# Optimization experiments

Hardware: AMD Instinct MI355X
Metric: run time of the kernel (lower is better)

The kernel has to match this reference:

```python
import jax, jax.numpy as jnp
import numpy as np

N_NODES = 100000
IN_DIM = 128
HID = 128
N_REL = 2
N_EDGES = 500000


def setup_inputs() -> dict:
    key = jax.random.key(0)
    ks = jax.random.split(key, 12)
    x = jax.random.normal(ks[0], (N_NODES, IN_DIM), dtype=jnp.float32)
    edge_index = jax.random.randint(ks[1], (2, N_EDGES), 0, N_NODES, dtype=jnp.int64)
    edge_type = jax.random.randint(ks[2], (N_EDGES,), 0, N_REL, dtype=jnp.int64)
    def w(k, shape, fan_in):
        return jax.random.normal(k, shape, dtype=jnp.float32) / np.sqrt(fan_in)
    return {
        "x": x,
        "edge_index": edge_index,
        "edge_type": edge_type,
        "W_rel1": w(ks[3], (N_REL, IN_DIM, HID), IN_DIM),
        "W_root1": w(ks[4], (IN_DIM, HID), IN_DIM),
        "b1": jnp.zeros((HID,), jnp.float32),
        "W_rel2": w(ks[5], (N_REL, HID, HID), HID),
        "W_root2": w(ks[6], (HID, HID), HID),
        "b2": jnp.zeros((HID,), jnp.float32),
        "Wc": w(ks[7], (HID, 2), HID),
        "bc": jnp.zeros((2,), jnp.float32),
    }


def rgcn_conv(x, src, dst, edge_type, W_rel, W_root, b, n_nodes):
    """PyG RGCNConv: out_i = x_i @ W_root + b + sum_r mean_{j in N_r(i)} x_j @ W_r."""
    out = x @ W_root + b
    for r in range(W_rel.shape[0]):  # small fixed relation count
        mask = (edge_type == r).astype(x.dtype)  # [E]
        xr = x @ W_rel[r]                         # [N, dout] transform-then-gather
        msg = xr[src] * mask[:, None]             # [E, dout]
        agg = jax.ops.segment_sum(msg, dst, num_segments=n_nodes)   # [N, dout]
        cnt = jax.ops.segment_sum(mask, dst, num_segments=n_nodes)  # [N]
        out = out + agg / jnp.maximum(cnt, 1.0)[:, None]            # mean aggr
    return out


def reference(x, edge_index, edge_type, W_rel1, W_root1, b1, W_rel2, W_root2, b2, Wc, bc):
    n = x.shape[0]
    src, dst = edge_index[0], edge_index[1]
    h = rgcn_conv(x, src, dst, edge_type, W_rel1, W_root1, b1, n)
    h = jax.nn.relu(h)
    # dropout is identity at inference (training=False)
    h = rgcn_conv(h, src, dst, edge_type, W_rel2, W_root2, b2, n)
    h = jax.nn.relu(h)
    logits = h @ Wc + bc
    return logits
```

## Files before the change

kernel.cpp:

```cpp
#include <hip/hip_runtime.h>
#include <hip/hip_fp16.h>

#define N_NODES 100000
#define PAD_N   100096
#define IN_DIM 128
#define HID 128
#define N_REL 2
#define N_EDGES 500000
#define M_SEG (N_REL * N_NODES)
#define SCAN_BLK 1024
#define SCAN_NB ((M_SEG + SCAN_BLK - 1) / SCAN_BLK)

#define CVT_BLOCKS 12500
#define PACK_BLOCKS 48
#define HIST_BLOCKS 1954

typedef __attribute__((ext_vector_type(8))) _Float16 half8;
typedef __attribute__((ext_vector_type(4))) float float4v;

__device__ __forceinline__ unsigned short f2h(float f) {
    return __half_as_ushort(__float2half(f));
}

__global__ __launch_bounds__(256) void prep_kernel(
    const float* __restrict__ X, unsigned short* __restrict__ Xb,
    const float* __restrict__ Wroot1, const float* __restrict__ Wrel1,
    const float* __restrict__ Wroot2, const float* __restrict__ Wrel2,
    unsigned short* __restrict__ Wp,
    const int* __restrict__ ei, const int* __restrict__ et,
    unsigned* __restrict__ cnt)
{
    int bid = blockIdx.x;
    if (bid < CVT_BLOCKS) {
        int i = bid * 256 + threadIdx.x;
        if (i >= N_NODES * IN_DIM / 4) return;
        float4 v = ((const float4*)X)[i];
        ushort4 o;
        o.x = f2h(v.x); o.y = f2h(v.y); o.z = f2h(v.z); o.w = f2h(v.w);
        ((ushort4*)Xb)[i] = o;
    } else if (bid < CVT_BLOCKS + PACK_BLOCKS) {
        int tid = (bid - CVT_BLOCKS) * 256 + threadIdx.x;
        int layer = tid / 6144;
        int rem   = tid % 6144;
        int ks    = rem / 512;
        int rem2  = rem % 512;
        int nt    = rem2 / 64;
        int lane  = rem2 % 64;
        int seg = ks >> 2;
        int kl  = (ks & 3) * 32 + (lane >> 4) * 8;
        int chan = nt * 16 + (lane & 15);
        const float* Wroot = layer ? Wroot2 : Wroot1;
        const float* Wrel  = layer ? Wrel2  : Wrel1;
        const float* W = (seg == 0) ? Wroot : (Wrel + (size_t)(seg - 1) * 128 * 128);
        unsigned short* dst = Wp + (size_t)tid * 8;
        #pragma unroll
        for (int j = 0; j < 8; ++j)
            dst[j] = f2h(W[(size_t)(kl + j) * 128 + chan]);
    } else {
        int e = (bid - CVT_BLOCKS - PACK_BLOCKS) * 256 + threadIdx.x;
        if (e >= N_EDGES) return;
        int dst = ei[N_EDGES + e];
        int r = et[e];
        atomicAdd(cnt + (size_t)r * N_NODES + dst, 1u);
    }
}

__global__ __launch_bounds__(256) void scan1_kernel(
    const unsigned* __restrict__ cnt,
    unsigned* __restrict__ rs, unsigned* __restrict__ bsums)
{
    __shared__ unsigned sdata[256];
    int t = threadIdx.x;
    int base = blockIdx.x * SCAN_BLK + t * 4;
    unsigned v[4]; unsigned s = 0;
    #pragma unroll
    for (int j = 0; j < 4; ++j) {
        v[j] = (base + j < M_SEG) ? cnt[base + j] : 0u;
        s += v[j];
    }
    sdata[t] = s;
    __syncthreads();
    #pragma unroll
    for (int off = 1; off < 256; off <<= 1) {
        unsigned x = (t >= off) ? sdata[t - off] : 0u;
        __syncthreads();
        if (t >= off) sdata[t] += x;
        __syncthreads();
    }
    unsigned excl = (t > 0) ? sdata[t - 1] : 0u;
    if (t == 255) bsums[blockIdx.x] = sdata[255];
    unsigned run = excl;
    #pragma unroll
    for (int j = 0; j < 4; ++j) {
        if (base + j < M_SEG) rs[base + j] = run;
        run += v[j];
    }
}

__global__ __launch_bounds__(256) void scan2_kernel(unsigned* __restrict__ bsums)
{
    __shared__ unsigned sdata[256];
    int t = threadIdx.x;
    sdata[t] = (t < SCAN_NB) ? bsums[t] : 0u;
    __syncthreads();
    #pragma unroll
    for (int off = 1; off < 256; off <<= 1) {
        unsigned x = (t >= off) ? sdata[t - off] : 0u;
        __syncthreads();
        if (t >= off) sdata[t] += x;
        __syncthreads();
    }
    if (t < SCAN_NB) bsums[t] = (t > 0) ? sdata[t - 1] : 0u;
}

__global__ __launch_bounds__(256) void scan3_kernel(
    unsigned* __restrict__ rs, const unsigned* __restrict__ bsums,
    unsigned* __restrict__ cursor)
{
    int i = blockIdx.x * blockDim.x + threadIdx.x;
    if (i < M_SEG) {
        unsigned v = rs[i] + bsums[i >> 10];
        rs[i] = v;
        cursor[i] = v;
    }
    if (i == 0) rs[M_SEG] = N_EDGES;
}

__global__ __launch_bounds__(256) void fill_kernel(
    const int* __restrict__ ei, const int* __restrict__ et,
    unsigned* __restrict__ cursor, unsigned* __restrict__ csr)
{
    int e = blockIdx.x * blockDim.x + threadIdx.x;
    if (e >= N_EDGES) return;
    int src = ei[e];
    int dst = ei[N_EDGES + e];
    int r = et[e];
    unsigned pos = atomicAdd(cursor + (size_t)r * N_NODES + dst, 1u);
    csr[pos] = (unsigned)src;
}

template <bool FINAL>
__global__ __launch_bounds__(256) void gemm_kernel(
    const unsigned short* __restrict__ Xin,
    const unsigned* __restrict__ rs,
    const unsigned* __restrict__ csr,
    const unsigned short* __restrict__ Wp,
    const float* __restrict__ bias,
    unsigned short* __restrict__ Hout,
    const float* __restrict__ Wc,
    const float* __restrict__ bc,
    float* __restrict__ Out)
{
    const int t    = threadIdx.x;
    const int w    = t >> 6;
    const int lane = t & 63;
    const int l15  = lane & 15;
    const int quad = lane >> 4;
    const int rowbase = blockIdx.x * 128 + w * 32;
    const int koff = quad * 8;

    const uint4* __restrict__ X4 = (const uint4*)Xin;

    unsigned p_[4], e_[4]; float inv_[4];
    #pragma unroll
    for (int r = 0; r < 2; ++r) {
        #pragma unroll
        for (int mt = 0; mt < 2; ++mt) {
            int c = r * 2 + mt;
            int node = rowbase + mt * 16 + l15;
            unsigned st = 0, en = 0;
            if (node < N_NODES) {
                unsigned sg = (unsigned)r * N_NODES + (unsigned)node;
                st = rs[sg];
                en = rs[sg + 1];
            }
            p_[c] = st; e_[c] = en;
            unsigned cdeg = en - st;
            inv_[c] = 1.0f / (float)(cdeg > 0u ? cdeg : 1u);
        }
    }

    __half2 a2[4][4][4];
    #pragma unroll
    for (int c = 0; c < 4; ++c)
        #pragma unroll
        for (int ksl = 0; ksl < 4; ++ksl)
            #pragma unroll
            for (int j = 0; j < 4; ++j)
                a2[c][ksl][j] = __float2half2_rn(0.f);

    const __half2 one2  = __float2half2_rn(1.f);
    const __half2 zero2 = __float2half2_rn(0.f);

    while (true) {
        bool act[4];
        bool anyl = false;
        #pragma unroll
        for (int c = 0; c < 4; ++c) { act[c] = p_[c] < e_[c]; anyl |= act[c]; }
        if (!__any(anyl)) break;

        unsigned s_[4];
        #pragma unroll
        for (int c = 0; c < 4; ++c)
            s_[c] = csr[act[c] ? p_[c] : 0u];

        uint4 v_[4][4];
        #pragma unroll
        for (int c = 0; c < 4; ++c) {
            const uint4* row = X4 + ((size_t)(act[c] ? s_[c] : 0u) << 4) + quad;
            v_[c][0] = row[0];
            v_[c][1] = row[4];
            v_[c][2] = row[8];
            v_[c][3] = row[12];
        }

        #pragma unroll
        for (int c = 0; c < 4; ++c) {
            __half2 m = act[c] ? one2 : zero2;
            #pragma unroll
            for (int ksl = 0; ksl < 4; ++ksl)
                #pragma unroll
                for (int j = 0; j < 4; ++j)
                    a2[c][ksl][j] = __hfma2(((const __half2*)&v_[c][ksl])[j], m,
                                            a2[c][ksl][j]);
            p_[c] += act[c] ? 1u : 0u;
        }
    }

    half8 ag[2][2][4];
    #pragma unroll
    for (int r = 0; r < 2; ++r)
        #pragma unroll
        for (int mt = 0; mt < 2; ++mt) {
            int c = r * 2 + mt;
            __half2 s2 = __float2half2_rn(inv_[c]);
            #pragma unroll
            for (int ksl = 0; ksl < 4; ++ksl) {
                half8 h;
                #pragma unroll
                for (int j = 0; j < 4; ++j)
                    ((__half2*)&h)[j] = __hmul2(a2[c][ksl][j], s2);
                ag[r][mt][ksl] = h;
            }
        }

    auto ldB = [&](int ks, int nt) -> half8 {
        return *(const half8*)(Wp + ((size_t)(ks * 8 + nt) * 64 + lane) * 8);
    };
    const unsigned short* aBase0 = Xin + (size_t)(rowbase + l15) * 128 + koff;
    const unsigned short* aBase1 = aBase0 + 16 * 128;
    auto ldA = [&](int ks, int mt) -> half8 {
        return *(const half8*)((mt ? aBase1 : aBase0) + (ks & 3) * 32);
    };

    float4v acc[2][8];
    #pragma unroll
    for (int nt = 0; nt < 8; ++nt) {
        float bv = bias[nt * 16 + l15];
        #pragma unroll
        for (int mt = 0; mt < 2; ++mt)
            acc[mt][nt] = float4v{bv, bv, bv, bv};
    }

    half8 bb[2][8];
    half8 aa[2][2];
    #pragma unroll
    for (int nt = 0; nt < 8; ++nt) bb[0][nt] = ldB(0, nt);
    aa[0][0] = ldA(0, 0);
    aa[0][1] = ldA(0, 1);

    #pragma unroll
    for (int ks = 0; ks < 12; ++ks) {
        if (ks + 1 < 12) {
            #pragma unroll
            for (int nt = 0; nt < 8; ++nt)
                bb[(ks + 1) & 1][nt] = ldB(ks + 1, nt);
            if (ks + 1 < 4) {
                aa[(ks + 1) & 1][0] = ldA(ks + 1, 0);
                aa[(ks + 1) & 1][1] = ldA(ks + 1, 1);
            }
        }
        half8 A0 = (ks < 4) ? aa[ks & 1][0] : ag[(ks >> 2) - 1][0][ks & 3];
        half8 A1 = (ks < 4) ? aa[ks & 1][1] : ag[(ks >> 2) - 1][1][ks & 3];
        #pragma unroll
        for (int nt = 0; nt < 8; ++nt) {
            acc[0][nt] = __builtin_amdgcn_mfma_f32_16x16x32_f16(A0, bb[ks & 1][nt], acc[0][nt], 0, 0, 0);
            acc[1][nt] = __builtin_amdgcn_mfma_f32_16x16x32_f16(A1, bb[ks & 1][nt], acc[1][nt], 0, 0, 0);
        }
    }

    if (!FINAL) {
        #pragma unroll
        for (int mt = 0; mt < 2; ++mt) {
            #pragma unroll
            for (int r = 0; r < 4; ++r) {
                int node = rowbase + mt * 16 + quad * 4 + r;
                unsigned short* hp = Hout + (size_t)node * 128 + l15;
                #pragma unroll
                for (int nt = 0; nt < 8; ++nt)
                    hp[nt * 16] = f2h(fmaxf(acc[mt][nt][r], 0.f));
            }
        }
    } else {
        float wc0[8], wc1[8];
        #pragma unroll
        for (int nt = 0; nt < 8; ++nt) {
            wc0[nt] = Wc[(nt * 16 + l15) * 2 + 0];
            wc1[nt] = Wc[(nt * 16 + l15) * 2 + 1];
        }
        float b0 = bc[0], b1 = bc[1];
        #pragma unroll
        for (int mt = 0; mt < 2; ++mt) {
            #pragma unroll
            for (int r = 0; r < 4; ++r) {
                float l0 = 0.f, l1 = 0.f;
                #pragma unroll
                for (int nt = 0; nt < 8; ++nt) {
                    float h = fmaxf(acc[mt][nt][r], 0.f);
                    l0 += h * wc0[nt];
                    l1 += h * wc1[nt];
                }
                #pragma unroll
                for (int off = 8; off > 0; off >>= 1) {
                    l0 += __shfl_down(l0, off, 16);
                    l1 += __shfl_down(l1, off, 16);
                }
                int node = rowbase + mt * 16 + quad * 4 + r;
                if (l15 == 0 && node < N_NODES) {
                    Out[(size_t)node * 2 + 0] = l0 + b0;
                    Out[(size_t)node * 2 + 1] = l1 + b1;
                }
            }
        }
    }
}

extern "C" void kernel_launch(void* const* d_in, const int* in_sizes, int n_in,
                              void* d_out, int out_size, void* d_ws, size_t ws_size,
                              hipStream_t stream)
{
    const float* x      = (const float*)d_in[0];
    const int*   ei     = (const int*)d_in[1];
    const int*   et     = (const int*)d_in[2];
    const float* Wrel1  = (const float*)d_in[3];
    const float* Wroot1 = (const float*)d_in[4];
    const float* b1     = (const float*)d_in[5];
    const float* Wrel2  = (const float*)d_in[6];
    const float* Wroot2 = (const float*)d_in[7];
    const float* b2     = (const float*)d_in[8];
    const float* Wc     = (const float*)d_in[9];
    const float* bc     = (const float*)d_in[10];
    float* out = (float*)d_out;

    char* ws = (char*)d_ws;
    size_t off = 0;
    auto alloc = [&](size_t bytes) {
        void* p = ws + off;
        off += (bytes + 255) & ~(size_t)255;
        return p;
    };
    unsigned short* xb    = (unsigned short*)alloc((size_t)PAD_N * IN_DIM * 2);
    unsigned short* h1b   = (unsigned short*)alloc((size_t)PAD_N * HID * 2);
    unsigned short* Wp    = (unsigned short*)alloc((size_t)2 * 12 * 8 * 64 * 8 * 2);
    unsigned*       rs    = (unsigned*)alloc((size_t)(M_SEG + 1) * 4);
    unsigned*       cursor= (unsigned*)alloc((size_t)M_SEG * 4);
    unsigned*       bsums = (unsigned*)alloc(256 * 4);
    unsigned*       csr   = (unsigned*)alloc((size_t)N_EDGES * 4);

    const int edge_blocks = (N_EDGES + 255) / 256;
    const int seg_blocks  = (M_SEG + 255) / 256;
    const int gemm_blocks = PAD_N / 128;
    const int prep_blocks = CVT_BLOCKS + PACK_BLOCKS + HIST_BLOCKS;

    hipMemsetAsync(cursor, 0, (size_t)M_SEG * 4, stream);
    prep_kernel<<<prep_blocks, 256, 0, stream>>>(
        x, xb, Wroot1, Wrel1, Wroot2, Wrel2, Wp, ei, et, cursor);
    scan1_kernel<<<SCAN_NB, 256, 0, stream>>>(cursor, rs, bsums);
    scan2_kernel<<<1, 256, 0, stream>>>(bsums);
    scan3_kernel<<<seg_blocks, 256, 0, stream>>>(rs, bsums, cursor);
    fill_kernel<<<edge_blocks, 256, 0, stream>>>(ei, et, cursor, csr);

    gemm_kernel<false><<<gemm_blocks, 256, 0, stream>>>(
        xb, rs, csr, Wp, b1, h1b, nullptr, nullptr, nullptr);

    gemm_kernel<true><<<gemm_blocks, 256, 0, stream>>>(
        h1b, rs, csr, Wp + (size_t)12 * 8 * 64 * 8, b2, nullptr, Wc, bc, out);
}
```

Before: 271.3 us.

## Halve rows per warp and software-pipeline CSR index loads in gather loop

Each warp now handles 16 nodes instead of 32, doubling the number of gemm blocks, and the neighbor-gather loop processes two edges per relation per iteration while prefetching the next iteration's CSR indices. This is meant to cut per-warp load imbalance and register pressure and to hide the dependent csr-then-row load latency. The cost is that each B weight fragment is reused by one MFMA tile instead of two, which doubles weight traffic per node, and wasted lanes can rise on odd degrees.

```diff
diff --git a/kernel.cpp b/kernel.cpp
--- a/kernel.cpp
+++ b/kernel.cpp
@@ -156,118 +156,138 @@
     const int lane = t & 63;
     const int l15  = lane & 15;
     const int quad = lane >> 4;
-    const int rowbase = blockIdx.x * 128 + w * 32;
+    const int rowbase = blockIdx.x * 64 + w * 16;
     const int koff = quad * 8;
 
     const uint4* __restrict__ X4 = (const uint4*)Xin;
 
-    unsigned p_[4], e_[4]; float inv_[4];
+    const int node = rowbase + l15;
+    unsigned p_[2], e_[2]; float inv_[2];
     #pragma unroll
     for (int r = 0; r < 2; ++r) {
-        #pragma unroll
-        for (int mt = 0; mt < 2; ++mt) {
-            int c = r * 2 + mt;
-            int node = rowbase + mt * 16 + l15;
-            unsigned st = 0, en = 0;
-            if (node < N_NODES) {
-                unsigned sg = (unsigned)r * N_NODES + (unsigned)node;
-                st = rs[sg];
-                en = rs[sg + 1];
-            }
-            p_[c] = st; e_[c] = en;
-            unsigned cdeg = en - st;
-            inv_[c] = 1.0f / (float)(cdeg > 0u ? cdeg : 1u);
-        }
-    }
-
-    __half2 a2[4][4][4];
-    #pragma unroll
-    for (int c = 0; c < 4; ++c)
+        unsigned st = 0, en = 0;
+        if (node < N_NODES) {
+            unsigned sg = (unsigned)r * N_NODES + (unsigned)node;
+            st = rs[sg];
+            en = rs[sg + 1];
+        }
+        p_[r] = st; e_[r] = en;
+        unsigned d = en - st;
+        inv_[r] = 1.0f / (float)(d ? d : 1u);
+    }
+
+    __half2 a2[2][4][4];
+    #pragma unroll
+    for (int r = 0; r < 2; ++r)
         #pragma unroll
         for (int ksl = 0; ksl < 4; ++ksl)
             #pragma unroll
             for (int j = 0; j < 4; ++j)
-                a2[c][ksl][j] = __float2half2_rn(0.f);
+                a2[r][ksl][j] = __float2half2_rn(0.f);
 
     const __half2 one2  = __float2half2_rn(1.f);
     const __half2 zero2 = __float2half2_rn(0.f);
 
-    while (true) {
-        bool act[4];
-        bool anyl = false;
-        #pragma unroll
-        for (int c = 0; c < 4; ++c) { act[c] = p_[c] < e_[c]; anyl |= act[c]; }
-        if (!__any(anyl)) break;
-
-        unsigned s_[4];
-        #pragma unroll
-        for (int c = 0; c < 4; ++c)
-            s_[c] = csr[act[c] ? p_[c] : 0u];
-
-        uint4 v_[4][4];
-        #pragma unroll
-        for (int c = 0; c < 4; ++c) {
-            const uint4* row = X4 + ((size_t)(act[c] ? s_[c] : 0u) << 4) + quad;
-            v_[c][0] = row[0];
-            v_[c][1] = row[4];
-            v_[c][2] = row[8];
-            v_[c][3] = row[12];
-        }
-
-        #pragma unroll
-        for (int c = 0; c < 4; ++c) {
-            __half2 m = act[c] ? one2 : zero2;
-            #pragma unroll
-            for (int ksl = 0; ksl < 4; ++ksl)
+    unsigned id[2][2];
+    #pragma unroll
+    for (int r = 0; r < 2; ++r)
+        #pragma unroll
+        for (int s = 0; s < 2; ++s) {
+            unsigned q = p_[r] + (unsigned)s;
+            id[r][s] = csr[q < e_[r] ? q : 0u];
+        }
+
+    while (__any((p_[0] < e_[0]) | (p_[1] < e_[1]))) {
+        bool act[2][2];
+        #pragma unroll
+        for (int r = 0; r < 2; ++r)
+            #pragma unroll
+            for (int s = 0; s < 2; ++s)
+                act[r][s] = (p_[r] + (unsigned)s) < e_[r];
+
+        uint4 v[2][2][4];
+        #pragma unroll
+        for (int r = 0; r < 2; ++r)
+            #pragma unroll
+            for (int s = 0; s < 2; ++s) {
+                const uint4* row = X4 +
+                    ((size_t)(act[r][s] ? id[r][s] : 0u) << 4) + quad;
+                v[r][s][0] = row[0];
+                v[r][s][1] = row[4];
+                v[r][s][2] = row[8];
+                v[r][s][3] = row[12];
+            }
+
+        unsigned pn[2];
+        #pragma unroll
+        for (int r = 0; r < 2; ++r) {
+            unsigned q = p_[r] + 2u;
+            pn[r] = q > e_[r] ? e_[r] : q;
+        }
+        unsigned idn[2][2];
+        #pragma unroll
+        for (int r = 0; r < 2; ++r)
+            #pragma unroll
+            for (int s = 0; s < 2; ++s) {
+                unsigned q = pn[r] + (unsigned)s;
+                idn[r][s] = csr[q < e_[r] ? q : 0u];
+            }
+
+        #pragma unroll
+        for (int r = 0; r < 2; ++r)
+            #pragma unroll
+            for (int s = 0; s < 2; ++s) {
+                __half2 m = act[r][s] ? one2 : zero2;
                 #pragma unroll
-                for (int j = 0; j < 4; ++j)
-                    a2[c][ksl][j] = __hfma2(((const __half2*)&v_[c][ksl])[j], m,
-                                            a2[c][ksl][j]);
-            p_[c] += act[c] ? 1u : 0u;
-        }
-    }
-
-    half8 ag[2][2][4];
-    #pragma unroll
-    for (int r = 0; r < 2; ++r)
-        #pragma unroll
-        for (int mt = 0; mt < 2; ++mt) {
-            int c = r * 2 + mt;
-            __half2 s2 = __float2half2_rn(inv_[c]);
-            #pragma unroll
-            for (int ksl = 0; ksl < 4; ++ksl) {
-                half8 h;
-                #pragma unroll
-                for (int j = 0; j < 4; ++j)
-                    ((__half2*)&h)[j] = __hmul2(a2[c][ksl][j], s2);
-                ag[r][mt][ksl] = h;
-            }
-        }
+                for (int ksl = 0; ksl < 4; ++ksl)
+                    #pragma unroll
+                    for (int j = 0; j < 4; ++j)
+                        a2[r][ksl][j] = __hfma2(((const __half2*)&v[r][s][ksl])[j],
+                                                m, a2[r][ksl][j]);
+            }
+
+        #pragma unroll
+        for (int r = 0; r < 2; ++r) {
+            p_[r] = pn[r];
+            #pragma unroll
+            for (int s = 0; s < 2; ++s) id[r][s] = idn[r][s];
+        }
+    }
+
+    half8 ag[2][4];
+    #pragma unroll
+    for (int r = 0; r < 2; ++r) {
+        __half2 s2 = __float2half2_rn(inv_[r]);
+        #pragma unroll
+        for (int ksl = 0; ksl < 4; ++ksl) {
+            half8 h;
+            #pragma unroll
+            for (int j = 0; j < 4; ++j)
+                ((__half2*)&h)[j] = __hmul2(a2[r][ksl][j], s2);
+            ag[r][ksl] = h;
+        }
+    }
 
     auto ldB = [&](int ks, int nt) -> half8 {
         return *(const half8*)(Wp + ((size_t)(ks * 8 + nt) * 64 + lane) * 8);
     };
-    const unsigned short* aBase0 = Xin + (size_t)(rowbase + l15) * 128 + koff;
-    const unsigned short* aBase1 = aBase0 + 16 * 128;
-    auto ldA = [&](int ks, int mt) -> half8 {
-        return *(const half8*)((mt ? aBase1 : aBase0) + (ks & 3) * 32);
+    const unsigned short* aBase = Xin + (size_t)(rowbase + l15) * 128 + koff;
+    auto ldA = [&](int ks) -> half8 {
+        return *(const half8*)(aBase + (ks & 3) * 32);
     };
 
-    float4v acc[2][8];
+    float4v acc[8];
     #pragma unroll
     for (int nt = 0; nt < 8; ++nt) {
         float bv = bias[nt * 16 + l15];
-        #pragma unroll
-        for (int mt = 0; mt < 2; ++mt)
-            acc[mt][nt] = float4v{bv, bv, bv, bv};
+        acc[nt] = float4v{bv, bv, bv, bv};
     }
 
     half8 bb[2][8];
-    half8 aa[2][2];
+    half8 ax[2];
     #pragma unroll
     for (int nt = 0; nt < 8; ++nt) bb[0][nt] = ldB(0, nt);
-    aa[0][0] = ldA(0, 0);
-    aa[0][1] = ldA(0, 1);
+    ax[0] = ldA(0);
 
     #pragma unroll
     for (int ks = 0; ks < 12; ++ks) {
@@ -275,31 +295,22 @@
             #pragma unroll
             for (int nt = 0; nt < 8; ++nt)
                 bb[(ks + 1) & 1][nt] = ldB(ks + 1, nt);
-            if (ks + 1 < 4) {
-                aa[(ks + 1) & 1][0] = ldA(ks + 1, 0);
-                aa[(ks + 1) & 1][1] = ldA(ks + 1, 1);
-            }
-        }
-        half8 A0 = (ks < 4) ? aa[ks & 1][0] : ag[(ks >> 2) - 1][0][ks & 3];
-        half8 A1 = (ks < 4) ? aa[ks & 1][1] : ag[(ks >> 2) - 1][1][ks & 3];
-        #pragma unroll
-        for (int nt = 0; nt < 8; ++nt) {
-            acc[0][nt] = __builtin_amdgcn_mfma_f32_16x16x32_f16(A0, bb[ks & 1][nt], acc[0][nt], 0, 0, 0);
-            acc[1][nt] = __builtin_amdgcn_mfma_f32_16x16x32_f16(A1, bb[ks & 1][nt], acc[1][nt], 0, 0, 0);
-        }
+            if (ks + 1 < 4) ax[(ks + 1) & 1] = ldA(ks + 1);
+        }
+        half8 A = (ks < 4) ? ax[ks & 1] : ag[(ks >> 2) - 1][ks & 3];
+        #pragma unroll
+        for (int nt = 0; nt < 8; ++nt)
+            acc[nt] = __builtin_amdgcn_mfma_f32_16x16x32_f16(A, bb[ks & 1][nt], acc[nt], 0, 0, 0);
     }
 
     if (!FINAL) {
         #pragma unroll
-        for (int mt = 0; mt < 2; ++mt) {
-            #pragma unroll
-            for (int r = 0; r < 4; ++r) {
-                int node = rowbase + mt * 16 + quad * 4 + r;
-                unsigned short* hp = Hout + (size_t)node * 128 + l15;
-                #pragma unroll
-                for (int nt = 0; nt < 8; ++nt)
-                    hp[nt * 16] = f2h(fmaxf(acc[mt][nt][r], 0.f));
-            }
+        for (int rr = 0; rr < 4; ++rr) {
+            int n2 = rowbase + quad * 4 + rr;
+            unsigned short* hp = Hout + (size_t)n2 * 128 + l15;
+            #pragma unroll
+            for (int nt = 0; nt < 8; ++nt)
+                hp[nt * 16] = f2h(fmaxf(acc[nt][rr], 0.f));
         }
     } else {
         float wc0[8], wc1[8];
@@ -310,26 +321,23 @@
         }
         float b0 = bc[0], b1 = bc[1];
         #pragma unroll
-        for (int mt = 0; mt < 2; ++mt) {
-            #pragma unroll
-            for (int r = 0; r < 4; ++r) {
-                float l0 = 0.f, l1 = 0.f;
-                #pragma unroll
-                for (int nt = 0; nt < 8; ++nt) {
-                    float h = fmaxf(acc[mt][nt][r], 0.f);
-                    l0 += h * wc0[nt];
-                    l1 += h * wc1[nt];
-                }
-                #pragma unroll
-                for (int off = 8; off > 0; off >>= 1) {
-                    l0 += __shfl_down(l0, off, 16);
-                    l1 += __shfl_down(l1, off, 16);
-                }
-                int node = rowbase + mt * 16 + quad * 4 + r;
-                if (l15 == 0 && node < N_NODES) {
-                    Out[(size_t)node * 2 + 0] = l0 + b0;
-                    Out[(size_t)node * 2 + 1] = l1 + b1;
-                }
+        for (int rr = 0; rr < 4; ++rr) {
+            float l0 = 0.f, l1 = 0.f;
+            #pragma unroll
+            for (int nt = 0; nt < 8; ++nt) {
+                float h = fmaxf(acc[nt][rr], 0.f);
+                l0 += h * wc0[nt];
+                l1 += h * wc1[nt];
+            }
+            #pragma unroll
+            for (int off = 8; off > 0; off >>= 1) {
+                l0 += __shfl_down(l0, off, 16);
+                l1 += __shfl_down(l1, off, 16);
+            }
+            int n2 = rowbase + quad * 4 + rr;
+            if (l15 == 0 && n2 < N_NODES) {
+                Out[(size_t)n2 * 2 + 0] = l0 + b0;
+                Out[(size_t)n2 * 2 + 1] = l1 + b1;
             }
         }
     }
@@ -369,7 +377,7 @@
 
     const int edge_blocks = (N_EDGES + 255) / 256;
     const int seg_blocks  = (M_SEG + 255) / 256;
-    const int gemm_blocks = PAD_N / 128;
+    const int gemm_blocks = PAD_N / 64;
     const int prep_blocks = CVT_BLOCKS + PACK_BLOCKS + HIST_BLOCKS;
 
     hipMemsetAsync(cursor, 0, (size_t)M_SEG * 4, stream);
```

Result: no change. 268.6 us (-1.0%).
